# Performance work log

Measured on AMD Instinct MI355X. Metric: run time of the kernel, lower is better.

## Reference

```python
import jax, jax.numpy as jnp
import numpy as np

N_NODES = 50000
N_EDGES = 600000
IN_DIM = 128
OUT_DIM = 128


def setup_inputs() -> dict:
    key = jax.random.key(0)
    k1, k2, k3, k4 = jax.random.split(key, 4)
    feature = jax.random.normal(k1, (N_NODES, IN_DIM), dtype=jnp.float32)
    W = jax.random.normal(k2, (IN_DIM, OUT_DIM), dtype=jnp.float32) * 0.05
    b = jnp.zeros((OUT_DIM,), dtype=jnp.float32)
    src = jax.random.randint(k3, (N_EDGES,), 0, N_NODES, dtype=jnp.int64 if jax.config.jax_enable_x64 else jnp.int32)
    dst = jax.random.randint(k4, (N_EDGES,), 0, N_NODES, dtype=jnp.int64 if jax.config.jax_enable_x64 else jnp.int32)
    return {"feature": feature, "W": W, "b": b, "src": src, "dst": dst}


def reference(feature, W, b, src, dst):
    # DGL GraphConv, norm='both' (eval mode => dropout is identity):
    #   out = relu( D_in^{-1/2} * A @ (D_out^{-1/2} * X) @ W + b )
    # degrees are clamped to a minimum of 1 as in DGL.
    n = feature.shape[0]
    ones = jnp.ones(src.shape[0], dtype=feature.dtype)
    out_deg = jnp.clip(jax.ops.segment_sum(ones, src, num_segments=n), 1.0)  # [N]
    in_deg = jnp.clip(jax.ops.segment_sum(ones, dst, num_segments=n), 1.0)   # [N]
    h = feature * jax.lax.rsqrt(out_deg)[:, None]                 # [N, in]
    agg = jax.ops.segment_sum(h[src], dst, num_segments=n)        # gather-scatter [N, in]
    agg = agg * jax.lax.rsqrt(in_deg)[:, None]
    out = agg @ W + b                                             # [N, out]
    return jax.nn.relu(out)
```

## Files before the change

kernel.cpp:

```cpp
#include <hip/hip_runtime.h>

constexpr int NODES = 50000;
constexpr int EDGES = 600000;
constexpr int DIM = 128;
constexpr int CHUNK = 1024;
constexpr int NB_SCAN = (NODES + CHUNK - 1) / CHUNK;
constexpr int HBINS = 8192;
constexpr int HRANGES = (NODES + HBINS - 1) / HBINS;
constexpr int HC = 40;
constexpr int EPC = EDGES / HC;
constexpr int EPC4 = EPC / 4;

typedef __attribute__((ext_vector_type(8))) short short8v;
typedef __attribute__((ext_vector_type(8))) unsigned short ushort8v;
typedef __attribute__((ext_vector_type(4))) float f32x4;

__device__ __forceinline__ unsigned short f2bf(float f) {
    unsigned int b = __float_as_uint(f);
    b += 0x7fffu + ((b >> 16) & 1u);
    return (unsigned short)(b >> 16);
}

__device__ __forceinline__ int swz(int row, int oct) {
    return row * 256 + ((oct ^ (row & 7)) << 4);
}

__global__ __launch_bounds__(256) void transpose_w(const float* __restrict__ W,
                                                   unsigned short* __restrict__ Wt) {
    int t = blockIdx.x * 256 + threadIdx.x;
    int n = t >> 7, k = t & 127;
    Wt[t] = f2bf(W[k * DIM + n]);
}

__global__ __launch_bounds__(256) void hist_kernel(const int* __restrict__ src,
                                                   const int* __restrict__ dst,
                                                   unsigned short* __restrict__ partial) {
    __shared__ int h[HBINS];
    int b = blockIdx.x;
    int arr = b / (HRANGES * HC);
    int rc  = b % (HRANGES * HC);
    int r = rc / HC, c = rc % HC;
    int tid = threadIdx.x;
    for (int i = tid; i < HBINS; i += 256) h[i] = 0;
    __syncthreads();
    const int4* idx = reinterpret_cast<const int4*>(arr == 0 ? src : dst);
    int t0 = c * EPC4;
    int base = r * HBINS;
    for (int t = t0 + tid; t < t0 + EPC4; t += 256) {
        int4 v = idx[t];
        int a0 = v.x - base; if ((unsigned)a0 < (unsigned)HBINS) atomicAdd(&h[a0], 1);
        int a1 = v.y - base; if ((unsigned)a1 < (unsigned)HBINS) atomicAdd(&h[a1], 1);
        int a2 = v.z - base; if ((unsigned)a2 < (unsigned)HBINS) atomicAdd(&h[a2], 1);
        int a3 = v.w - base; if ((unsigned)a3 < (unsigned)HBINS) atomicAdd(&h[a3], 1);
    }
    __syncthreads();
    unsigned short* outp = partial + (size_t)b * HBINS;
    for (int i = tid; i < HBINS; i += 256) outp[i] = (unsigned short)h[i];
}

__global__ __launch_bounds__(256) void deg_coff(const unsigned short* __restrict__ partial,
                                                int* __restrict__ deg_out,
                                                int* __restrict__ deg_in,
                                                unsigned short* __restrict__ cumoff) {
    int n = blockIdx.x * 256 + threadIdx.x;
    if (n >= HRANGES * HBINS) return;
    int r = n >> 13, bin = n & (HBINS - 1);
    const unsigned short* ps = partial;
    const unsigned short* pd = partial + (size_t)HRANGES * HC * HBINS;
    int s0 = 0, run = 0;
    #pragma unroll 8
    for (int c = 0; c < HC; ++c) {
        size_t idx = (size_t)(r * HC + c) * HBINS + bin;
        s0 += ps[idx];
        cumoff[idx] = (unsigned short)run;
        run += pd[idx];
    }
    if (n < NODES) {
        deg_out[n] = s0;
        deg_in[n] = run;
    }
}

__global__ __launch_bounds__(256) void scan_partials(const int* __restrict__ deg_in,
                                                     int* __restrict__ scan_part) {
    __shared__ int wsum[4];
    int tid = threadIdx.x, lane = tid & 63, wid = tid >> 6;
    int base = blockIdx.x * CHUNK + tid * 4;
    int s = 0;
    #pragma unroll
    for (int i = 0; i < 4; ++i)
        if (base + i < NODES) s += deg_in[base + i];
    #pragma unroll
    for (int off = 32; off; off >>= 1) s += __shfl_down(s, off, 64);
    if (lane == 0) wsum[wid] = s;
    __syncthreads();
    if (tid == 0)
        scan_part[blockIdx.x] = wsum[0] + wsum[1] + wsum[2] + wsum[3];
}

__global__ __launch_bounds__(256) void scan_chunks(const int* __restrict__ deg_in,
                                                   const int* __restrict__ scan_part,
                                                   int* __restrict__ row_start) {
    __shared__ int wsum[4];
    __shared__ int blockoff_s;
    int b = blockIdx.x, tid = threadIdx.x, lane = tid & 63, wid = tid >> 6;
    if (wid == 0) {
        int v = (lane < b) ? scan_part[lane] : 0;
        #pragma unroll
        for (int off = 32; off; off >>= 1) v += __shfl_down(v, off, 64);
        if (lane == 0) blockoff_s = v;
    }
    int base = b * CHUNK + tid * 4;
    int v[4];
    int s = 0;
    #pragma unroll
    for (int i = 0; i < 4; ++i) {
        v[i] = (base + i < NODES) ? deg_in[base + i] : 0;
        s += v[i];
    }
    int incl = s;
    #pragma unroll
    for (int off = 1; off < 64; off <<= 1) {
        int t = __shfl_up(incl, off, 64);
        if (lane >= off) incl += t;
    }
    if (lane == 63) wsum[wid] = incl;
    __syncthreads();
    int wbase = 0;
    for (int w = 0; w < wid; ++w) wbase += wsum[w];
    int run = blockoff_s + wbase + incl - s;
    #pragma unroll
    for (int i = 0; i < 4; ++i) {
        if (base + i < NODES) row_start[base + i] = run;
        run += v[i];
    }
}

__global__ __launch_bounds__(256) void bucket_lds(const int* __restrict__ src,
                                                  const int* __restrict__ dst,
                                                  const int* __restrict__ row_start,
                                                  const unsigned short* __restrict__ cumoff,
                                                  int* __restrict__ csr_src) {
    __shared__ int cur[HBINS];
    int r = blockIdx.x / HC, c = blockIdx.x % HC;
    int tid = threadIdx.x;
    int base = r * HBINS;
    const unsigned short* co = cumoff + (size_t)(r * HC + c) * HBINS;
    for (int i = tid; i < HBINS; i += 256) {
        int n = base + i;
        int rs = (n < NODES) ? row_start[n] : 0;
        cur[i] = rs + (int)co[i];
    }
    __syncthreads();
    const int4* dst4 = reinterpret_cast<const int4*>(dst);
    const int4* src4 = reinterpret_cast<const int4*>(src);
    int t0 = c * EPC4;
    for (int t = t0 + tid; t < t0 + EPC4; t += 256) {
        int4 dv = dst4[t];
        int4 sv = src4[t];
        int d;
        d = dv.x - base; if ((unsigned)d < (unsigned)HBINS) csr_src[atomicAdd(&cur[d], 1)] = sv.x;
        d = dv.y - base; if ((unsigned)d < (unsigned)HBINS) csr_src[atomicAdd(&cur[d], 1)] = sv.y;
        d = dv.z - base; if ((unsigned)d < (unsigned)HBINS) csr_src[atomicAdd(&cur[d], 1)] = sv.z;
        d = dv.w - base; if ((unsigned)d < (unsigned)HBINS) csr_src[atomicAdd(&cur[d], 1)] = sv.w;
    }
}

__global__ __launch_bounds__(256) void gemm_mfma(const float* __restrict__ X,
                                                 const int* __restrict__ deg_out,
                                                 const unsigned short* __restrict__ Wt,
                                                 unsigned short* __restrict__ H) {
    __shared__ char XsB[64 * 256];
    __shared__ char WsB[128 * 256];
    int tid = threadIdx.x;
    int row0 = blockIdx.x * 64;

    for (int t = tid; t < 128 * 16; t += 256) {
        int n = t >> 4, o = t & 15;
        ushort8v wv = *reinterpret_cast<const ushort8v*>(Wt + n * DIM + o * 8);
        *reinterpret_cast<ushort8v*>(WsB + swz(n, o)) = wv;
    }
    for (int t = tid; t < 64 * 16; t += 256) {
        int r = t >> 4, o = t & 15;
        int node = row0 + r;
        float4 v0 = make_float4(0.f, 0.f, 0.f, 0.f), v1 = v0;
        float sc = 0.f;
        if (node < NODES) {
            const float4* rp = reinterpret_cast<const float4*>(X + (size_t)node * DIM);
            v0 = rp[o * 2];
            v1 = rp[o * 2 + 1];
            int dg = deg_out[node];
            sc = rsqrtf((float)(dg > 0 ? dg : 1));
        }
        ushort8v h;
        h[0] = f2bf(v0.x * sc); h[1] = f2bf(v0.y * sc);
        h[2] = f2bf(v0.z * sc); h[3] = f2bf(v0.w * sc);
        h[4] = f2bf(v1.x * sc); h[5] = f2bf(v1.y * sc);
        h[6] = f2bf(v1.z * sc); h[7] = f2bf(v1.w * sc);
        *reinterpret_cast<ushort8v*>(XsB + swz(r, o)) = h;
    }
    __syncthreads();

    int w = tid >> 6, l = tid & 63;
    int lr = l & 15, lg = l >> 4;
    f32x4 acc[8];
    #pragma unroll
    for (int nt = 0; nt < 8; ++nt) acc[nt] = (f32x4){0.f, 0.f, 0.f, 0.f};
    #pragma unroll
    for (int kb = 0; kb < 4; ++kb) {
        short8v a = *reinterpret_cast<short8v*>(XsB + swz(w * 16 + lr, kb * 4 + lg));
        #pragma unroll
        for (int nt = 0; nt < 8; ++nt) {
            short8v bfr = *reinterpret_cast<short8v*>(WsB + swz(nt * 16 + lr, kb * 4 + lg));
            acc[nt] = __builtin_amdgcn_mfma_f32_16x16x32_bf16(a, bfr, acc[nt], 0, 0, 0);
        }
    }
    #pragma unroll
    for (int nt = 0; nt < 8; ++nt) {
        int col = nt * 16 + lr;
        #pragma unroll
        for (int rg = 0; rg < 4; ++rg) {
            int m = w * 16 + lg * 4 + rg;
            int byte = m * 256 + (((col >> 3) ^ (m & 7)) << 4) + (col & 7) * 2;
            *reinterpret_cast<unsigned short*>(XsB + byte) = f2bf(acc[nt][rg]);
        }
    }
    __syncthreads();
    for (int t = tid; t < 64 * 16; t += 256) {
        int r = t >> 4, o = t & 15;
        int node = row0 + r;
        if (node < NODES)
            *reinterpret_cast<ushort8v*>(H + (size_t)node * DIM + o * 8) =
                *reinterpret_cast<ushort8v*>(XsB + swz(r, o));
    }
}

__global__ __launch_bounds__(256) void gather_kernel(const unsigned int* __restrict__ Hu,
                                                     const int* __restrict__ row_start,
                                                     const int* __restrict__ deg_in,
                                                     const int* __restrict__ csr_src,
                                                     const float* __restrict__ bias,
                                                     float* __restrict__ out) {
    int gw = (blockIdx.x * 256 + threadIdx.x) >> 6;
    int lane = threadIdx.x & 63;
    if (gw >= NODES) return;
    int start = row_start[gw];
    int deg = deg_in[gw];
    float ax = 0.f, ay = 0.f;
    for (int i0 = 0; i0 < deg; i0 += 64) {
        int nv = min(64, deg - i0);
        int sv = 0;
        if (i0 + lane < deg) sv = csr_src[start + i0 + lane];
        int i = 0;
        for (; i + 4 <= nv; i += 4) {
            int s0 = __shfl(sv, i, 64);
            int s1 = __shfl(sv, i + 1, 64);
            int s2 = __shfl(sv, i + 2, 64);
            int s3 = __shfl(sv, i + 3, 64);
            unsigned int u0 = Hu[(size_t)s0 * 64 + lane];
            unsigned int u1 = Hu[(size_t)s1 * 64 + lane];
            unsigned int u2 = Hu[(size_t)s2 * 64 + lane];
            unsigned int u3 = Hu[(size_t)s3 * 64 + lane];
            ax += __uint_as_float(u0 << 16);
            ay += __uint_as_float(u0 & 0xffff0000u);
            ax += __uint_as_float(u1 << 16);
            ay += __uint_as_float(u1 & 0xffff0000u);
            ax += __uint_as_float(u2 << 16);
            ay += __uint_as_float(u2 & 0xffff0000u);
            ax += __uint_as_float(u3 << 16);
            ay += __uint_as_float(u3 & 0xffff0000u);
        }
        for (; i < nv; ++i) {
            int s = __shfl(sv, i, 64);
            unsigned int u = Hu[(size_t)s * 64 + lane];
            ax += __uint_as_float(u << 16);
            ay += __uint_as_float(u & 0xffff0000u);
        }
    }
    float sc = rsqrtf((float)(deg > 0 ? deg : 1));
    float2 bb = reinterpret_cast<const float2*>(bias)[lane];
    float2 o;
    o.x = fmaxf(ax * sc + bb.x, 0.f);
    o.y = fmaxf(ay * sc + bb.y, 0.f);
    reinterpret_cast<float2*>(out)[(size_t)gw * 64 + lane] = o;
}

extern "C" void kernel_launch(void* const* d_in, const int* in_sizes, int n_in,
                              void* d_out, int out_size, void* d_ws, size_t ws_size,
                              hipStream_t stream) {
    const float* feat = (const float*)d_in[0];
    const float* W    = (const float*)d_in[1];
    const float* b    = (const float*)d_in[2];
    const int*   src  = (const int*)d_in[3];
    const int*   dst  = (const int*)d_in[4];
    float* out = (float*)d_out;

    constexpr size_t PART_ELEMS = (size_t)HRANGES * HC * HBINS;

    char* p = (char*)d_ws;
    unsigned short* partial = (unsigned short*)p;
    unsigned short* cumoff  = partial + 2 * PART_ELEMS;
    unsigned short* H       = (unsigned short*)p;
    p += 3 * PART_ELEMS * sizeof(unsigned short);
    unsigned short* Wt = (unsigned short*)p;  p += (size_t)DIM * DIM * 2;
    int* deg_out   = (int*)p;  p += (size_t)NODES * 4;
    int* deg_in    = (int*)p;  p += (size_t)NODES * 4;
    int* row_start = (int*)p;  p += (size_t)NODES * 4;
    int* scan_part = (int*)p;  p += 256;
    int* csr_src   = (int*)p;

    transpose_w<<<DIM * DIM / 256, 256, 0, stream>>>(W, Wt);
    hist_kernel<<<2 * HRANGES * HC, 256, 0, stream>>>(src, dst, partial);
    deg_coff<<<(HRANGES * HBINS) / 256, 256, 0, stream>>>(partial, deg_out, deg_in, cumoff);
    scan_partials<<<NB_SCAN, 256, 0, stream>>>(deg_in, scan_part);
    scan_chunks<<<NB_SCAN, 256, 0, stream>>>(deg_in, scan_part, row_start);
    bucket_lds<<<HRANGES * HC, 256, 0, stream>>>(src, dst, row_start, cumoff, csr_src);
    gemm_mfma<<<(NODES + 63) / 64, 256, 0, stream>>>(feat, deg_out, Wt, H);
    gather_kernel<<<(NODES * 64 + 255) / 256, 256, 0, stream>>>(
        (const unsigned int*)H, row_start, deg_in, csr_src, b, out);
}
```

Baseline: 164.7 us.

## Fuse prep kernels, fold scan partials into deg_coff, widen gather to half-wave edges

Transpose of W and both histograms move into one prep kernel, and each block now counts src and dst together. The separate scan_partials kernel is removed; deg_coff accumulates chunk sums into scan_part with atomics, and prep zeroes scan_part. The gather kernel now lets each half-wave take a different edge and load 8 bytes per lane, then combines the halves with a cross-half shuffle. The goal is fewer launches and more edges in flight during the gather, at the cost of doubled LDS per histogram block and an ordering dependency on the zeroing of scan_part.

Result: no change. 166.6 us (+1.1%).

```diff
diff --git a/kernel.cpp b/kernel.cpp
--- a/kernel.cpp
+++ b/kernel.cpp
@@ -10,6 +10,7 @@
 constexpr int HC = 40;
 constexpr int EPC = EDGES / HC;
 constexpr int EPC4 = EPC / 4;
+constexpr int TW_BLOCKS = DIM * DIM / 256;
 
 typedef __attribute__((ext_vector_type(8))) short short8v;
 typedef __attribute__((ext_vector_type(8))) unsigned short ushort8v;
@@ -25,45 +26,61 @@
     return row * 256 + ((oct ^ (row & 7)) << 4);
 }
 
-__global__ __launch_bounds__(256) void transpose_w(const float* __restrict__ W,
-                                                   unsigned short* __restrict__ Wt) {
-    int t = blockIdx.x * 256 + threadIdx.x;
-    int n = t >> 7, k = t & 127;
-    Wt[t] = f2bf(W[k * DIM + n]);
-}
-
-__global__ __launch_bounds__(256) void hist_kernel(const int* __restrict__ src,
+__global__ __launch_bounds__(256) void prep_kernel(const float* __restrict__ W,
+                                                   const int* __restrict__ src,
                                                    const int* __restrict__ dst,
-                                                   unsigned short* __restrict__ partial) {
-    __shared__ int h[HBINS];
+                                                   unsigned short* __restrict__ Wt,
+                                                   unsigned short* __restrict__ partial,
+                                                   int* __restrict__ scan_part) {
+    __shared__ int hs[HBINS];
+    __shared__ int hd[HBINS];
     int b = blockIdx.x;
-    int arr = b / (HRANGES * HC);
-    int rc  = b % (HRANGES * HC);
-    int r = rc / HC, c = rc % HC;
     int tid = threadIdx.x;
-    for (int i = tid; i < HBINS; i += 256) h[i] = 0;
-    __syncthreads();
-    const int4* idx = reinterpret_cast<const int4*>(arr == 0 ? src : dst);
+    if (b < TW_BLOCKS) {
+        int t = b * 256 + tid;
+        int n = t >> 7, k = t & 127;
+        Wt[t] = f2bf(W[k * DIM + n]);
+        if (b == 0 && tid < 64) scan_part[tid] = 0;
+        return;
+    }
+    b -= TW_BLOCKS;
+    int r = b / HC, c = b % HC;
+    for (int i = tid; i < HBINS; i += 256) { hs[i] = 0; hd[i] = 0; }
+    __syncthreads();
+    const int4* s4 = reinterpret_cast<const int4*>(src);
+    const int4* d4 = reinterpret_cast<const int4*>(dst);
     int t0 = c * EPC4;
     int base = r * HBINS;
     for (int t = t0 + tid; t < t0 + EPC4; t += 256) {
-        int4 v = idx[t];
-        int a0 = v.x - base; if ((unsigned)a0 < (unsigned)HBINS) atomicAdd(&h[a0], 1);
-        int a1 = v.y - base; if ((unsigned)a1 < (unsigned)HBINS) atomicAdd(&h[a1], 1);
-        int a2 = v.z - base; if ((unsigned)a2 < (unsigned)HBINS) atomicAdd(&h[a2], 1);
-        int a3 = v.w - base; if ((unsigned)a3 < (unsigned)HBINS) atomicAdd(&h[a3], 1);
-    }
-    __syncthreads();
-    unsigned short* outp = partial + (size_t)b * HBINS;
-    for (int i = tid; i < HBINS; i += 256) outp[i] = (unsigned short)h[i];
+        int4 v = s4[t];
+        int a;
+        a = v.x - base; if ((unsigned)a < (unsigned)HBINS) atomicAdd(&hs[a], 1);
+        a = v.y - base; if ((unsigned)a < (unsigned)HBINS) atomicAdd(&hs[a], 1);
+        a = v.z - base; if ((unsigned)a < (unsigned)HBINS) atomicAdd(&hs[a], 1);
+        a = v.w - base; if ((unsigned)a < (unsigned)HBINS) atomicAdd(&hs[a], 1);
+        int4 w = d4[t];
+        a = w.x - base; if ((unsigned)a < (unsigned)HBINS) atomicAdd(&hd[a], 1);
+        a = w.y - base; if ((unsigned)a < (unsigned)HBINS) atomicAdd(&hd[a], 1);
+        a = w.z - base; if ((unsigned)a < (unsigned)HBINS) atomicAdd(&hd[a], 1);
+        a = w.w - base; if ((unsigned)a < (unsigned)HBINS) atomicAdd(&hd[a], 1);
+    }
+    __syncthreads();
+    unsigned short* ops = partial + (size_t)(r * HC + c) * HBINS;
+    unsigned short* opd = ops + (size_t)HRANGES * HC * HBINS;
+    for (int i = tid; i < HBINS; i += 256) {
+        ops[i] = (unsigned short)hs[i];
+        opd[i] = (unsigned short)hd[i];
+    }
 }
 
 __global__ __launch_bounds__(256) void deg_coff(const unsigned short* __restrict__ partial,
                                                 int* __restrict__ deg_out,
                                                 int* __restrict__ deg_in,
-                                                unsigned short* __restrict__ cumoff) {
-    int n = blockIdx.x * 256 + threadIdx.x;
-    if (n >= HRANGES * HBINS) return;
+                                                unsigned short* __restrict__ cumoff,
+                                                int* __restrict__ scan_part) {
+    __shared__ int bsum[4];
+    int tid = threadIdx.x;
+    int n = blockIdx.x * 256 + tid;
     int r = n >> 13, bin = n & (HBINS - 1);
     const unsigned short* ps = partial;
     const unsigned short* pd = partial + (size_t)HRANGES * HC * HBINS;
@@ -79,23 +96,14 @@
         deg_out[n] = s0;
         deg_in[n] = run;
     }
-}
-
-__global__ __launch_bounds__(256) void scan_partials(const int* __restrict__ deg_in,
-                                                     int* __restrict__ scan_part) {
-    __shared__ int wsum[4];
-    int tid = threadIdx.x, lane = tid & 63, wid = tid >> 6;
-    int base = blockIdx.x * CHUNK + tid * 4;
-    int s = 0;
-    #pragma unroll
-    for (int i = 0; i < 4; ++i)
-        if (base + i < NODES) s += deg_in[base + i];
-    #pragma unroll
-    for (int off = 32; off; off >>= 1) s += __shfl_down(s, off, 64);
-    if (lane == 0) wsum[wid] = s;
+    int lane = tid & 63, wid = tid >> 6;
+    int v = (n < NODES) ? run : 0;
+    #pragma unroll
+    for (int off = 32; off; off >>= 1) v += __shfl_down(v, off, 64);
+    if (lane == 0) bsum[wid] = v;
     __syncthreads();
     if (tid == 0)
-        scan_part[blockIdx.x] = wsum[0] + wsum[1] + wsum[2] + wsum[3];
+        atomicAdd(&scan_part[blockIdx.x >> 2], bsum[0] + bsum[1] + bsum[2] + bsum[3]);
 }
 
 __global__ __launch_bounds__(256) void scan_chunks(const int* __restrict__ deg_in,
@@ -235,7 +243,7 @@
     }
 }
 
-__global__ __launch_bounds__(256) void gather_kernel(const unsigned int* __restrict__ Hu,
+__global__ __launch_bounds__(256) void gather_kernel(const uint2* __restrict__ H2,
                                                      const int* __restrict__ row_start,
                                                      const int* __restrict__ deg_in,
                                                      const int* __restrict__ csr_src,
@@ -244,45 +252,63 @@
     int gw = (blockIdx.x * 256 + threadIdx.x) >> 6;
     int lane = threadIdx.x & 63;
     if (gw >= NODES) return;
+    int half = lane >> 5;
+    int sub = lane & 31;
     int start = row_start[gw];
     int deg = deg_in[gw];
-    float ax = 0.f, ay = 0.f;
+    float ax = 0.f, ay = 0.f, az = 0.f, aw = 0.f;
     for (int i0 = 0; i0 < deg; i0 += 64) {
         int nv = min(64, deg - i0);
         int sv = 0;
         if (i0 + lane < deg) sv = csr_src[start + i0 + lane];
         int i = 0;
-        for (; i + 4 <= nv; i += 4) {
-            int s0 = __shfl(sv, i, 64);
-            int s1 = __shfl(sv, i + 1, 64);
-            int s2 = __shfl(sv, i + 2, 64);
-            int s3 = __shfl(sv, i + 3, 64);
-            unsigned int u0 = Hu[(size_t)s0 * 64 + lane];
-            unsigned int u1 = Hu[(size_t)s1 * 64 + lane];
-            unsigned int u2 = Hu[(size_t)s2 * 64 + lane];
-            unsigned int u3 = Hu[(size_t)s3 * 64 + lane];
-            ax += __uint_as_float(u0 << 16);
-            ay += __uint_as_float(u0 & 0xffff0000u);
-            ax += __uint_as_float(u1 << 16);
-            ay += __uint_as_float(u1 & 0xffff0000u);
-            ax += __uint_as_float(u2 << 16);
-            ay += __uint_as_float(u2 & 0xffff0000u);
-            ax += __uint_as_float(u3 << 16);
-            ay += __uint_as_float(u3 & 0xffff0000u);
-        }
-        for (; i < nv; ++i) {
+        for (; i + 8 <= nv; i += 8) {
+            int s0 = __shfl(sv, i + half, 64);
+            int s1 = __shfl(sv, i + 2 + half, 64);
+            int s2 = __shfl(sv, i + 4 + half, 64);
+            int s3 = __shfl(sv, i + 6 + half, 64);
+            uint2 u0 = H2[(size_t)s0 * 32 + sub];
+            uint2 u1 = H2[(size_t)s1 * 32 + sub];
+            uint2 u2 = H2[(size_t)s2 * 32 + sub];
+            uint2 u3 = H2[(size_t)s3 * 32 + sub];
+            ax += __uint_as_float(u0.x << 16); ay += __uint_as_float(u0.x & 0xffff0000u);
+            az += __uint_as_float(u0.y << 16); aw += __uint_as_float(u0.y & 0xffff0000u);
+            ax += __uint_as_float(u1.x << 16); ay += __uint_as_float(u1.x & 0xffff0000u);
+            az += __uint_as_float(u1.y << 16); aw += __uint_as_float(u1.y & 0xffff0000u);
+            ax += __uint_as_float(u2.x << 16); ay += __uint_as_float(u2.x & 0xffff0000u);
+            az += __uint_as_float(u2.y << 16); aw += __uint_as_float(u2.y & 0xffff0000u);
+            ax += __uint_as_float(u3.x << 16); ay += __uint_as_float(u3.x & 0xffff0000u);
+            az += __uint_as_float(u3.y << 16); aw += __uint_as_float(u3.y & 0xffff0000u);
+        }
+        for (; i + 2 <= nv; i += 2) {
+            int s = __shfl(sv, i + half, 64);
+            uint2 u = H2[(size_t)s * 32 + sub];
+            ax += __uint_as_float(u.x << 16); ay += __uint_as_float(u.x & 0xffff0000u);
+            az += __uint_as_float(u.y << 16); aw += __uint_as_float(u.y & 0xffff0000u);
+        }
+        if (i < nv) {
             int s = __shfl(sv, i, 64);
-            unsigned int u = Hu[(size_t)s * 64 + lane];
-            ax += __uint_as_float(u << 16);
-            ay += __uint_as_float(u & 0xffff0000u);
-        }
-    }
-    float sc = rsqrtf((float)(deg > 0 ? deg : 1));
-    float2 bb = reinterpret_cast<const float2*>(bias)[lane];
-    float2 o;
-    o.x = fmaxf(ax * sc + bb.x, 0.f);
-    o.y = fmaxf(ay * sc + bb.y, 0.f);
-    reinterpret_cast<float2*>(out)[(size_t)gw * 64 + lane] = o;
+            if (half == 0) {
+                uint2 u = H2[(size_t)s * 32 + sub];
+                ax += __uint_as_float(u.x << 16); ay += __uint_as_float(u.x & 0xffff0000u);
+                az += __uint_as_float(u.y << 16); aw += __uint_as_float(u.y & 0xffff0000u);
+            }
+        }
+    }
+    ax += __shfl_xor(ax, 32, 64);
+    ay += __shfl_xor(ay, 32, 64);
+    az += __shfl_xor(az, 32, 64);
+    aw += __shfl_xor(aw, 32, 64);
+    if (half == 0) {
+        float sc = rsqrtf((float)(deg > 0 ? deg : 1));
+        float4 bb = reinterpret_cast<const float4*>(bias)[sub];
+        float4 o;
+        o.x = fmaxf(ax * sc + bb.x, 0.f);
+        o.y = fmaxf(ay * sc + bb.y, 0.f);
+        o.z = fmaxf(az * sc + bb.z, 0.f);
+        o.w = fmaxf(aw * sc + bb.w, 0.f);
+        reinterpret_cast<float4*>(out)[(size_t)gw * 32 + sub] = o;
+    }
 }
 
 extern "C" void kernel_launch(void* const* d_in, const int* in_sizes, int n_in,
@@ -309,13 +335,11 @@
     int* scan_part = (int*)p;  p += 256;
     int* csr_src   = (int*)p;
 
-    transpose_w<<<DIM * DIM / 256, 256, 0, stream>>>(W, Wt);
-    hist_kernel<<<2 * HRANGES * HC, 256, 0, stream>>>(src, dst, partial);
-    deg_coff<<<(HRANGES * HBINS) / 256, 256, 0, stream>>>(partial, deg_out, deg_in, cumoff);
-    scan_partials<<<NB_SCAN, 256, 0, stream>>>(deg_in, scan_part);
+    prep_kernel<<<TW_BLOCKS + HRANGES * HC, 256, 0, stream>>>(W, src, dst, Wt, partial, scan_part);
+    deg_coff<<<(HRANGES * HBINS) / 256, 256, 0, stream>>>(partial, deg_out, deg_in, cumoff, scan_part);
     scan_chunks<<<NB_SCAN, 256, 0, stream>>>(deg_in, scan_part, row_start);
     bucket_lds<<<HRANGES * HC, 256, 0, stream>>>(src, dst, row_start, cumoff, csr_src);
     gemm_mfma<<<(NODES + 63) / 64, 256, 0, stream>>>(feat, deg_out, Wt, H);
     gather_kernel<<<(NODES * 64 + 255) / 256, 256, 0, stream>>>(
-        (const unsigned int*)H, row_start, deg_in, csr_src, b, out);
-}
+        (const uint2*)H, row_start, deg_in, csr_src, b, out);
+}
```
